# Kernel tuning notes

Measured on AMD Instinct MI355X. Metric: run time of the kernel, lower is better.

The kernel has to match this reference:

```python
import jax, jax.numpy as jnp
import numpy as np

EPS = 1e-5

def _bn(x):
    # training-mode batchnorm (batch stats), gamma=1 beta=0 per the module's init
    ax = tuple(range(x.ndim - 1))
    m = x.mean(ax, keepdims=True)
    v = x.var(ax, keepdims=True)
    return (x - m) * jax.lax.rsqrt(v + EPS)

def _mlp(x, weights):
    # shared 1x1-conv MLP: pointwise linear -> BN -> ReLU
    for W in weights:
        x = jax.nn.relu(_bn(jnp.einsum('...c,oc->...o', x, W)))
    return x

def _fps_single(xyz, npoint):
    # farthest point sampling, xyz [N,3] -> [npoint] int32 indices
    N = xyz.shape[0]
    def step(carry, _):
        dists, far = carry
        d = jnp.sum((xyz - xyz[far]) ** 2, -1)
        dists = jnp.minimum(dists, d)
        return (dists, jnp.argmax(dists).astype(jnp.int32)), far
    init = (jnp.full((N,), 1e10, xyz.dtype), jnp.int32(0))
    _, idx = jax.lax.scan(step, init, None, length=npoint)
    return idx

def _ball_query(new_xyz, xyz, radius, nsample):
    # first nsample points (in original order) within radius of each center
    d2 = jnp.sum((new_xyz[:, :, None, :] - xyz[:, None, :, :]) ** 2, -1)  # [B,S,N]
    N = xyz.shape[1]
    rank = jnp.where(d2 < radius * radius, jnp.arange(N, dtype=jnp.int32), jnp.int32(N))
    vals, _ = jax.lax.top_k(-rank, nsample)
    idx = -vals
    idx = jnp.where(idx == N, idx[..., :1], idx)  # pad with first valid (center itself)
    return idx

def _gather(pts, idx):
    # pts [B,N,C], idx [B,S,ns] -> [B,S,ns,C]
    B, S, ns = idx.shape
    return jnp.take_along_axis(pts, idx.reshape(B, S * ns, 1), axis=1).reshape(B, S, ns, pts.shape[-1])

def _sa(xyz, feats, npoint, radius, nsample, weights):
    fps_idx = jax.vmap(_fps_single, in_axes=(0, None))(xyz, npoint)
    new_xyz = jnp.take_along_axis(xyz, fps_idx[:, :, None], axis=1)  # [B,S,3]
    idx = _ball_query(new_xyz, xyz, radius, nsample)
    g_xyz = (_gather(xyz, idx) - new_xyz[:, :, None, :]) / radius  # normalize_xyz
    x = g_xyz if feats is None else jnp.concatenate([g_xyz, _gather(feats, idx)], -1)
    x = _mlp(x, weights)
    return new_xyz, x.max(axis=2), fps_idx  # maxpool over nsample

def _forward(obj_cloud, gripper_cloud, sa1_w0, sa1_w1, sa1_w2, sa2_w0, sa2_w1, sa2_w2,
             sa3_w0, sa3_w1, sa3_w2, ge_w0, ge_w1, ge_w2,
             head_w0, head_b0, head_w1, head_b1, head_w2, head_b2):
    # gripper encoder: pointwise conv1d MLP + global maxpool
    g = _mlp(gripper_cloud, [ge_w0, ge_w1, ge_w2])      # [B,G,128]
    gripper_feature = g.max(axis=1)                      # [B,128]
    # backbone
    xyz1, f1, _ = _sa(obj_cloud, None, 512, 0.2, 32, [sa1_w0, sa1_w1, sa1_w2])
    xyz2, f2, _ = _sa(xyz1, f1, 128, 0.4, 64, [sa2_w0, sa2_w1, sa2_w2])
    # sa3: group_all (use_xyz, no centering/normalization)
    x = jnp.concatenate([xyz2, f2], -1)[:, None]         # [B,1,128,259]
    x = _mlp(x, [sa3_w0, sa3_w1, sa3_w2])
    obj_feature = x.max(axis=2)[:, 0]                    # [B,1024]
    comb = jnp.concatenate([gripper_feature, obj_feature], -1)  # [B,1152]
    h = _bn(comb)
    h = jax.nn.relu(_bn(h @ head_w0.T + head_b0))
    h = jax.nn.relu(_bn(h @ head_w1.T + head_b1))
    return jax.nn.relu(h @ head_w2.T + head_b2)          # [B,1]

def setup_inputs() -> dict:
    key = jax.random.key(0)
    ks = jax.random.split(key, 24)
    def w(k, o, i):
        return (jax.random.normal(k, (o, i), jnp.float32) * 0.05)
    inp = {
        'obj_cloud': jax.random.uniform(ks[0], (8, 20000, 3), jnp.float32),
        'gripper_cloud': jax.random.uniform(ks[1], (8, 512, 3), jnp.float32),
        'sa1_w0': w(ks[2], 64, 3),   'sa1_w1': w(ks[3], 64, 64),   'sa1_w2': w(ks[4], 128, 64),
        'sa2_w0': w(ks[5], 128, 131),'sa2_w1': w(ks[6], 128, 128), 'sa2_w2': w(ks[7], 256, 128),
        'sa3_w0': w(ks[8], 256, 259),'sa3_w1': w(ks[9], 512, 256), 'sa3_w2': w(ks[10], 1024, 512),
        'ge_w0': w(ks[11], 64, 3),   'ge_w1': w(ks[12], 128, 64),  'ge_w2': w(ks[13], 128, 128),
        'head_w0': w(ks[14], 512, 1152), 'head_b0': jnp.zeros((512,), jnp.float32),
        'head_w1': w(ks[15], 256, 512),  'head_b1': jnp.zeros((256,), jnp.float32),
        'head_w2': w(ks[16], 1, 256),    'head_b2': jnp.zeros((1,), jnp.float32),
    }
    return inp

def reference(obj_cloud, gripper_cloud, sa1_w0, sa1_w1, sa1_w2, sa2_w0, sa2_w1, sa2_w2,
              sa3_w0, sa3_w1, sa3_w2, ge_w0, ge_w1, ge_w2,
              head_w0, head_b0, head_w1, head_b1, head_w2, head_b2):
    return _forward(obj_cloud, gripper_cloud, sa1_w0, sa1_w1, sa1_w2, sa2_w0, sa2_w1, sa2_w2,
                    sa3_w0, sa3_w1, sa3_w2, ge_w0, ge_w1, ge_w2,
                    head_w0, head_b0, head_w1, head_b1, head_w2, head_b2)
```

## Files before the change

### kernel.cpp

```cpp
#include <hip/hip_runtime.h>
#include <cstddef>
#include <cstdint>

#define EPS_BN 1e-5f
#define NBINS 4
#define NEG_INF (-__builtin_inff())

template <bool FUSE_IN, bool FUSE_MAX>
__global__ __launch_bounds__(256) void gemm_xwt(const float* __restrict__ X,
                                                const float* __restrict__ Wm,
                                                float* __restrict__ Y,
                                                int R, int Cin, int Cout,
                                                const float* __restrict__ st_in, int Rin,
                                                float* __restrict__ st_out,
                                                float* __restrict__ pooled, int ns) {
  __shared__ __align__(16) float Xs[16][132];
  __shared__ __align__(16) float Ws[16][132];
  __shared__ float sMean[512], sScale[512];
  const int t  = threadIdx.x;
  const int r0 = blockIdx.x << 7;
  const int n0 = blockIdx.y << 7;
  const int tx = t & 15;
  const int ty = t >> 4;

  if constexpr (FUSE_IN) {
    const float inv = 1.f / (float)Rin;
    for (int k = t; k < Cin; k += 256) {
      float s = 0.f, q = 0.f;
#pragma unroll
      for (int bn = 0; bn < NBINS; ++bn) {
        s += st_in[bn * 2 * Cin + k];
        q += st_in[bn * 2 * Cin + Cin + k];
      }
      const float m  = s * inv;
      const float vr = fmaf(-m, m, q * inv);
      sMean[k]  = m;
      sScale[k] = rsqrtf(vr + EPS_BN);
    }
    __syncthreads();
  }

  float acc[8][8] = {};
  const int rStage = t >> 1;
  const int kBase  = (t & 1) << 3;
  const int nr     = n0 + rStage;

  for (int k0 = 0; k0 < Cin; k0 += 16) {
    const float* xrow = X  + (size_t)(r0 + rStage) * Cin + k0 + kBase;
    const float* wrow = Wm + (size_t)nr * Cin + k0 + kBase;
    if (((Cin & 3) == 0) && (k0 + 16 <= Cin)) {
      float4 xa = *(const float4*)(xrow);
      float4 xb = *(const float4*)(xrow + 4);
      if constexpr (FUSE_IN) {
        const int kb = k0 + kBase;
        xa.x = fmaxf(0.f, (xa.x - sMean[kb + 0]) * sScale[kb + 0]);
        xa.y = fmaxf(0.f, (xa.y - sMean[kb + 1]) * sScale[kb + 1]);
        xa.z = fmaxf(0.f, (xa.z - sMean[kb + 2]) * sScale[kb + 2]);
        xa.w = fmaxf(0.f, (xa.w - sMean[kb + 3]) * sScale[kb + 3]);
        xb.x = fmaxf(0.f, (xb.x - sMean[kb + 4]) * sScale[kb + 4]);
        xb.y = fmaxf(0.f, (xb.y - sMean[kb + 5]) * sScale[kb + 5]);
        xb.z = fmaxf(0.f, (xb.z - sMean[kb + 6]) * sScale[kb + 6]);
        xb.w = fmaxf(0.f, (xb.w - sMean[kb + 7]) * sScale[kb + 7]);
      }
      Xs[kBase + 0][rStage] = xa.x; Xs[kBase + 1][rStage] = xa.y;
      Xs[kBase + 2][rStage] = xa.z; Xs[kBase + 3][rStage] = xa.w;
      Xs[kBase + 4][rStage] = xb.x; Xs[kBase + 5][rStage] = xb.y;
      Xs[kBase + 6][rStage] = xb.z; Xs[kBase + 7][rStage] = xb.w;
      float4 wa = {0, 0, 0, 0}, wb = {0, 0, 0, 0};
      if (nr < Cout) { wa = *(const float4*)(wrow); wb = *(const float4*)(wrow + 4); }
      Ws[kBase + 0][rStage] = wa.x; Ws[kBase + 1][rStage] = wa.y;
      Ws[kBase + 2][rStage] = wa.z; Ws[kBase + 3][rStage] = wa.w;
      Ws[kBase + 4][rStage] = wb.x; Ws[kBase + 5][rStage] = wb.y;
      Ws[kBase + 6][rStage] = wb.z; Ws[kBase + 7][rStage] = wb.w;
    } else {
#pragma unroll
      for (int u = 0; u < 8; ++u) {
        const int k = k0 + kBase + u;
        float xe = 0.f, we = 0.f;
        if (k < Cin) {
          xe = xrow[u];
          if constexpr (FUSE_IN) xe = fmaxf(0.f, (xe - sMean[k]) * sScale[k]);
          if (nr < Cout) we = wrow[u];
        }
        Xs[kBase + u][rStage] = xe;
        Ws[kBase + u][rStage] = we;
      }
    }
    __syncthreads();
#pragma unroll
    for (int kk = 0; kk < 16; ++kk) {
      const float4 a0 = *(const float4*)(&Xs[kk][ty << 2]);
      const float4 a1 = *(const float4*)(&Xs[kk][64 + (ty << 2)]);
      const float4 b0 = *(const float4*)(&Ws[kk][tx << 2]);
      const float4 b1 = *(const float4*)(&Ws[kk][64 + (tx << 2)]);
      const float av[8] = {a0.x, a0.y, a0.z, a0.w, a1.x, a1.y, a1.z, a1.w};
      const float bw[8] = {b0.x, b0.y, b0.z, b0.w, b1.x, b1.y, b1.z, b1.w};
#pragma unroll
      for (int i = 0; i < 8; ++i)
#pragma unroll
        for (int j = 0; j < 8; ++j) acc[i][j] = fmaf(av[i], bw[j], acc[i][j]);
    }
    __syncthreads();
  }
  if constexpr (!FUSE_MAX) {
#pragma unroll
    for (int h = 0; h < 2; ++h)
#pragma unroll
      for (int i = 0; i < 4; ++i) {
        const int r = r0 + h * 64 + (ty << 2) + i;
        float* yr = Y + (size_t)r * Cout;
#pragma unroll
        for (int g = 0; g < 2; ++g) {
          const int n = n0 + g * 64 + (tx << 2);
          if (n < Cout) {
            float4 o = {acc[h * 4 + i][g * 4 + 0], acc[h * 4 + i][g * 4 + 1],
                        acc[h * 4 + i][g * 4 + 2], acc[h * 4 + i][g * 4 + 3]};
            *(float4*)(yr + n) = o;
          }
        }
      }
  }
#pragma unroll
  for (int g = 0; g < 2; ++g)
#pragma unroll
    for (int j = 0; j < 4; ++j) {
      float s = 0.f, q = 0.f;
#pragma unroll
      for (int rh = 0; rh < 8; ++rh) {
        const float v = acc[rh][g * 4 + j];
        s += v;
        q = fmaf(v, v, q);
      }
      Xs[ty][g * 64 + (tx << 2) + j] = s;
      Ws[ty][g * 64 + (tx << 2) + j] = q;
    }
  __syncthreads();
  if (t < 128) {
    const int n = n0 + t;
    if (n < Cout) {
      float s = 0.f, q = 0.f;
#pragma unroll
      for (int w = 0; w < 16; ++w) { s += Xs[w][t]; q += Ws[w][t]; }
      float* dst = st_out + (blockIdx.x & (NBINS - 1)) * 2 * Cout;
      atomicAdd(dst + n, s);
      atomicAdd(dst + Cout + n, q);
    }
  }
  if constexpr (FUSE_MAX) {
    __syncthreads();
    float mxAll = NEG_INF;
#pragma unroll
    for (int h = 0; h < 2; ++h) {
#pragma unroll
      for (int g2 = 0; g2 < 2; ++g2)
#pragma unroll
        for (int j = 0; j < 4; ++j) {
          float mx = acc[h * 4 + 0][g2 * 4 + j];
          mx = fmaxf(mx, acc[h * 4 + 1][g2 * 4 + j]);
          mx = fmaxf(mx, acc[h * 4 + 2][g2 * 4 + j]);
          mx = fmaxf(mx, acc[h * 4 + 3][g2 * 4 + j]);
          Xs[ty][g2 * 64 + (tx << 2) + j] = mx;
        }
      __syncthreads();
      if (t < 128) {
        const int n = n0 + t;
        if (n < Cout) {
          if (ns <= 64) {
            const int tpg = ns >> 2;
            const int gph = 64 / ns;
            for (int gq = 0; gq < gph; ++gq) {
              float mx = NEG_INF;
              for (int w = gq * tpg; w < gq * tpg + tpg; ++w) mx = fmaxf(mx, Xs[w][t]);
              const int g = (r0 + h * 64) / ns + gq;
              pooled[(size_t)g * Cout + n] = mx;
            }
          } else {
            float mx = NEG_INF;
            for (int w = 0; w < 16; ++w) mx = fmaxf(mx, Xs[w][t]);
            mxAll = fmaxf(mxAll, mx);
          }
        }
      }
      __syncthreads();
    }
    if (ns > 64 && t < 128) {
      const int n = n0 + t;
      if (n < Cout) pooled[(size_t)(r0 >> 7) * Cout + n] = mxAll;
    }
  }
}

__global__ void bn_apply_pooled(const float* __restrict__ P, const float* __restrict__ st,
                                float* __restrict__ o, int G, int C, int Rtrue) {
  const int i = blockIdx.x * 256 + threadIdx.x;
  if (i >= G * C) return;
  const int c = i % C;
  float s = 0.f, q = 0.f;
#pragma unroll
  for (int bn = 0; bn < NBINS; ++bn) {
    s += st[bn * 2 * C + c];
    q += st[bn * 2 * C + C + c];
  }
  const float inv = 1.f / (float)Rtrue;
  const float m  = s * inv;
  const float vr = fmaf(-m, m, q * inv);
  const float sc = rsqrtf(vr + EPS_BN);
  o[i] = fmaxf(0.f, (P[i] - m) * sc);
}

__global__ void bn_apply_relu_maxpool(const float* __restrict__ Y,
                                      const float* __restrict__ st,
                                      float* __restrict__ o, int G, int ns, int C) {
  const int i = blockIdx.x * 256 + threadIdx.x;
  if (i >= G * C) return;
  const int c = i % C;
  const int g = i / C;
  float s = 0.f, q = 0.f;
#pragma unroll
  for (int bn = 0; bn < NBINS; ++bn) {
    s += st[bn * 2 * C + c];
    q += st[bn * 2 * C + C + c];
  }
  const int R = G * ns;
  const float inv = 1.f / (float)R;
  const float m  = s * inv;
  const float vr = fmaf(-m, m, q * inv);
  const float sc = rsqrtf(vr + EPS_BN);
  const float* p = Y + (size_t)g * ns * C + c;
  float mx = NEG_INF;
  for (int k = 0; k < ns; ++k) mx = fmaxf(mx, p[(size_t)k * C]);
  o[i] = fmaxf(0.f, (mx - m) * sc);
}

#define REP20(X) X(0) X(1) X(2) X(3) X(4) X(5) X(6) X(7) X(8) X(9) \
                 X(10) X(11) X(12) X(13) X(14) X(15) X(16) X(17) X(18) X(19)

__global__ __launch_bounds__(1024)
__attribute__((amdgpu_waves_per_eu(4, 4)))
void fps_sa1_kernel(const float* __restrict__ xyz, float* __restrict__ new_xyz) {
  const int b    = blockIdx.x;
  const int tid  = threadIdx.x;
  const int lane = tid & 63;
  const int wave = tid >> 6;
  const float* p = xyz + (size_t)b * 20000 * 3;

  __shared__ float sv[16], sx[16], sy[16], sz[16];
  __shared__ int   si[16];
  __shared__ float bc[3];

#define DECLR(k) float px##k, py##k, pz##k, dd##k;
  REP20(DECLR)
#undef DECLR

#define INITR(k) {                                                          \
    const int i = tid + ((k) << 10);                                        \
    if (i < 20000) {                                                        \
      px##k = p[i * 3 + 0]; py##k = p[i * 3 + 1]; pz##k = p[i * 3 + 2];     \
      dd##k = 1e10f;                                                        \
    } else {                                                                \
      px##k = 0.f; py##k = 0.f; pz##k = 0.f;                                \
      dd##k = NEG_INF;                                                      \
    } }
  REP20(INITR)
#undef INITR

  float fx = p[0], fy = p[1], fz = p[2];
  if (tid == 0) {
    float* o = new_xyz + (size_t)b * 512 * 3;
    o[0] = fx; o[1] = fy; o[2] = fz;
  }
  __syncthreads();

  for (int s = 1; s < 512; ++s) {
    float bv = NEG_INF;
    int   bi = 0x7fffffff;
    float bx = 0.f, by = 0.f, bz = 0.f;
#define SCANR(k) {                                                          \
    const float dx = px##k - fx, dy = py##k - fy, dz = pz##k - fz;          \
    const float d  = __fadd_rn(__fadd_rn(__fmul_rn(dx, dx), __fmul_rn(dy, dy)), \
                               __fmul_rn(dz, dz));                          \
    const float nd = fminf(dd##k, d);                                       \
    dd##k = nd;                                                             \
    if (nd > bv) { bv = nd; bi = tid + ((k) << 10);                         \
                   bx = px##k; by = py##k; bz = pz##k; } }
    REP20(SCANR)
#undef SCANR
    float v  = bv;
    int   i0 = bi;
#pragma unroll
    for (int m = 1; m < 64; m <<= 1) {
      const float ov = __shfl_xor(v, m, 64);
      const int   oi = __shfl_xor(i0, m, 64);
      if (ov > v || (ov == v && oi < i0)) { v = ov; i0 = oi; }
    }
    if (i0 == bi) {
      sv[wave] = bv; si[wave] = bi; sx[wave] = bx; sy[wave] = by; sz[wave] = bz;
    }
    __syncthreads();
    if (tid < 64) {
      const float lv = (lane < 16) ? sv[lane] : NEG_INF;
      const int   li = (lane < 16) ? si[lane] : 0x7fffffff;
      float v2 = lv;
      int   i2 = li;
#pragma unroll
      for (int m = 1; m < 16; m <<= 1) {
        const float ov = __shfl_xor(v2, m, 64);
        const int   oi = __shfl_xor(i2, m, 64);
        if (ov > v2 || (ov == v2 && oi < i2)) { v2 = ov; i2 = oi; }
      }
      if (lane < 16 && li == i2) {
        const float wx = sx[lane], wy = sy[lane], wz = sz[lane];
        bc[0] = wx; bc[1] = wy; bc[2] = wz;
        float* o = new_xyz + ((size_t)b * 512 + s) * 3;
        o[0] = wx; o[1] = wy; o[2] = wz;
      }
    }
    __syncthreads();
    fx = bc[0]; fy = bc[1]; fz = bc[2];
  }
}

template <int N, int NP, int THREADS, int NPT>
__global__ __launch_bounds__(THREADS)
void fps2_kernel(const float* __restrict__ xyz, float* __restrict__ new_xyz) {
  constexpr int NW = THREADS / 64;
  const int b    = blockIdx.x;
  const int tid  = threadIdx.x;
  const int lane = tid & 63;
  const int wave = tid >> 6;
  const float* p = xyz + (size_t)b * N * 3;
  float px[NPT], py[NPT], pz[NPT], dd[NPT];
#pragma unroll
  for (int j = 0; j < NPT; ++j) {
    const int i = tid + j * THREADS;
    if (i < N) {
      px[j] = p[i * 3 + 0];
      py[j] = p[i * 3 + 1];
      pz[j] = p[i * 3 + 2];
      dd[j] = 1e10f;
    } else {
      px[j] = 0.f; py[j] = 0.f; pz[j] = 0.f;
      dd[j] = NEG_INF;
    }
  }
  __shared__ float sv[NW], sx[NW], sy[NW], sz[NW];
  __shared__ int   si[NW];
  __shared__ float bc[3];
  float fx = p[0], fy = p[1], fz = p[2];
  if (tid == 0) {
    float* o = new_xyz + (size_t)b * NP * 3;
    o[0] = fx; o[1] = fy; o[2] = fz;
  }
  for (int s = 1; s < NP; ++s) {
    float bv = NEG_INF;
    int   bi = 0x7fffffff;
    float bx = 0.f, by = 0.f, bz = 0.f;
#pragma unroll
    for (int j = 0; j < NPT; ++j) {
      const float dx = px[j] - fx;
      const float dy = py[j] - fy;
      const float dz = pz[j] - fz;
      const float d  = __fadd_rn(__fadd_rn(__fmul_rn(dx, dx), __fmul_rn(dy, dy)),
                                 __fmul_rn(dz, dz));
      const float nd = fminf(dd[j], d);
      dd[j] = nd;
      if (nd > bv) { bv = nd; bi = tid + j * THREADS; bx = px[j]; by = py[j]; bz = pz[j]; }
    }
    float v = bv;
    int   i0 = bi;
#pragma unroll
    for (int m = 1; m < 64; m <<= 1) {
      const float ov = __shfl_xor(v, m, 64);
      const int   oi = __shfl_xor(i0, m, 64);
      if (ov > v || (ov == v && oi < i0)) { v = ov; i0 = oi; }
    }
    if (i0 == bi) {
      sv[wave] = bv; si[wave] = bi; sx[wave] = bx; sy[wave] = by; sz[wave] = bz;
    }
    __syncthreads();
    if (tid < 64) {
      const float lv = (lane < NW) ? sv[lane] : NEG_INF;
      const int   li = (lane < NW) ? si[lane] : 0x7fffffff;
      float v2 = lv;
      int   i2 = li;
#pragma unroll
      for (int m = 1; m < NW; m <<= 1) {
        const float ov = __shfl_xor(v2, m, 64);
        const int   oi = __shfl_xor(i2, m, 64);
        if (ov > v2 || (ov == v2 && oi < i2)) { v2 = ov; i2 = oi; }
      }
      if (lane < NW && li == i2) {
        const float wx = sx[lane], wy = sy[lane], wz = sz[lane];
        bc[0] = wx; bc[1] = wy; bc[2] = wz;
        float* o = new_xyz + ((size_t)b * NP + s) * 3;
        o[0] = wx; o[1] = wy; o[2] = wz;
      }
    }
    __syncthreads();
    fx = bc[0]; fy = bc[1]; fz = bc[2];
  }
}

template <int N, int NS>
__global__ __launch_bounds__(256)
void ballquery_wave_kernel(const float* __restrict__ centers,
                           const float* __restrict__ pts,
                           int* __restrict__ idx, int BS, int S, float r2) {
  const int w    = (blockIdx.x * 256 + threadIdx.x) >> 6;
  const int lane = threadIdx.x & 63;
  if (w >= BS) return;
  const int b = w / S;
  const float cx = centers[w * 3 + 0];
  const float cy = centers[w * 3 + 1];
  const float cz = centers[w * 3 + 2];
  const float* p = pts + (size_t)b * N * 3;
  int* o = idx + (size_t)w * NS;
  int total = 0;
  int first = -1;
  for (int i0 = 0; i0 < N && total < NS; i0 += 64) {
    const int i = i0 + lane;
    bool pred = false;
    if (i < N) {
      const float dx = cx - p[i * 3 + 0];
      const float dy = cy - p[i * 3 + 1];
      const float dz = cz - p[i * 3 + 2];
      const float d2 = __fadd_rn(__fadd_rn(__fmul_rn(dx, dx), __fmul_rn(dy, dy)),
                                 __fmul_rn(dz, dz));
      pred = (d2 < r2);
    }
    const unsigned long long mask = __ballot(pred);
    if (mask) {
      const unsigned long long below = (lane == 0) ? 0ull : (mask << (64 - lane));
      const int before = __popcll(below);
      if (pred && (total + before) < NS) o[total + before] = i;
      if (first < 0) first = i0 + (__ffsll((long long)mask) - 1);
      total += __popcll(mask);
    }
  }
  if (lane >= total && lane < NS) o[lane] = first;
}

__global__ void group1_kernel(const float* __restrict__ xyz, const float* __restrict__ ctr,
                              const int* __restrict__ idx, float* __restrict__ X1) {
  const int t = blockIdx.x * 256 + threadIdx.x;
  if (t >= 8 * 512 * 32) return;
  const int g = t >> 5;
  const int b = g >> 9;
  const int i = idx[t];
  const float* p = xyz + ((size_t)b * 20000 + i) * 3;
  const float* c = ctr + (size_t)g * 3;
  X1[t * 3 + 0] = (p[0] - c[0]) / 0.2f;
  X1[t * 3 + 1] = (p[1] - c[1]) / 0.2f;
  X1[t * 3 + 2] = (p[2] - c[2]) / 0.2f;
}

__global__ void group2_kernel(const float* __restrict__ xyz1,
                              const float* __restrict__ xyz2,
                              const float* __restrict__ f1,
                              const int* __restrict__ idx2,
                              float* __restrict__ X2) {
  const int t = blockIdx.x * 256 + threadIdx.x;
  if (t >= 65536 * 131) return;
  const int r = t / 131;
  const int c = t - r * 131;
  const int g = r >> 6;
  const int b = g >> 7;
  const int i = idx2[r];
  float v;
  if (c < 3) {
    v = (xyz1[((size_t)b * 512 + i) * 3 + c] - xyz2[(size_t)g * 3 + c]) / 0.4f;
  } else {
    v = f1[((size_t)b * 512 + i) * 128 + (c - 3)];
  }
  X2[t] = v;
}

__global__ void build_x3_kernel(const float* __restrict__ xyz2, const float* __restrict__ f2,
                                float* __restrict__ X3) {
  const int t = blockIdx.x * 256 + threadIdx.x;
  if (t >= 1024 * 259) return;
  const int r = t / 259;
  const int c = t - r * 259;
  X3[t] = (c < 3) ? xyz2[r * 3 + c] : f2[(size_t)r * 256 + (c - 3)];
}

__global__ __launch_bounds__(512) void head_kernel(
    const float* __restrict__ gfeat, const float* __restrict__ objf,
    const float* __restrict__ w0, const float* __restrict__ b0,
    const float* __restrict__ w1, const float* __restrict__ b1,
    const float* __restrict__ w2, const float* __restrict__ b2,
    float* __restrict__ out) {
  __shared__ __align__(16) float comb[8 * 1152];
  __shared__ __align__(16) float h1[8 * 512];
  __shared__ __align__(16) float h2[8 * 256];
  const int tid = threadIdx.x;
  for (int i = tid; i < 8 * 1152; i += 512) {
    const int b = i / 1152, c = i - b * 1152;
    comb[i] = (c < 128) ? gfeat[b * 128 + c] : objf[b * 1024 + (c - 128)];
  }
  __syncthreads();
  for (int c = tid; c < 1152; c += 512) {
    float s = 0.f;
#pragma unroll
    for (int b = 0; b < 8; ++b) s += comb[b * 1152 + c];
    const float m = s * 0.125f;
    float v = 0.f;
#pragma unroll
    for (int b = 0; b < 8; ++b) { const float d = comb[b * 1152 + c] - m; v = fmaf(d, d, v); }
    const float sc = rsqrtf(v * 0.125f + EPS_BN);
#pragma unroll
    for (int b = 0; b < 8; ++b) comb[b * 1152 + c] = (comb[b * 1152 + c] - m) * sc;
  }
  __syncthreads();
  {
    float a[8];
#pragma unroll
    for (int b = 0; b < 8; ++b) a[b] = b0[tid];
    const float* wr = w0 + (size_t)tid * 1152;
    for (int ci = 0; ci < 1152; ci += 4) {
      const float4 wv = *(const float4*)(wr + ci);
#pragma unroll
      for (int b = 0; b < 8; ++b) {
        const float4 xv = *(const float4*)(&comb[b * 1152 + ci]);
        a[b] = fmaf(xv.x, wv.x, a[b]);
        a[b] = fmaf(xv.y, wv.y, a[b]);
        a[b] = fmaf(xv.z, wv.z, a[b]);
        a[b] = fmaf(xv.w, wv.w, a[b]);
      }
    }
    float s = 0.f;
#pragma unroll
    for (int b = 0; b < 8; ++b) s += a[b];
    const float m = s * 0.125f;
    float v = 0.f;
#pragma unroll
    for (int b = 0; b < 8; ++b) { const float d = a[b] - m; v = fmaf(d, d, v); }
    const float sc = rsqrtf(v * 0.125f + EPS_BN);
#pragma unroll
    for (int b = 0; b < 8; ++b) h1[b * 512 + tid] = fmaxf(0.f, (a[b] - m) * sc);
  }
  __syncthreads();
  if (tid < 256) {
    float a[8];
#pragma unroll
    for (int b = 0; b < 8; ++b) a[b] = b1[tid];
    const float* wr = w1 + (size_t)tid * 512;
    for (int ci = 0; ci < 512; ci += 4) {
      const float4 wv = *(const float4*)(wr + ci);
#pragma unroll
      for (int b = 0; b < 8; ++b) {
        const float4 xv = *(const float4*)(&h1[b * 512 + ci]);
        a[b] = fmaf(xv.x, wv.x, a[b]);
        a[b] = fmaf(xv.y, wv.y, a[b]);
        a[b] = fmaf(xv.z, wv.z, a[b]);
        a[b] = fmaf(xv.w, wv.w, a[b]);
      }
    }
    float s = 0.f;
#pragma unroll
    for (int b = 0; b < 8; ++b) s += a[b];
    const float m = s * 0.125f;
    float v = 0.f;
#pragma unroll
    for (int b = 0; b < 8; ++b) { const float d = a[b] - m; v = fmaf(d, d, v); }
    const float sc = rsqrtf(v * 0.125f + EPS_BN);
#pragma unroll
    for (int b = 0; b < 8; ++b) h2[b * 256 + tid] = fmaxf(0.f, (a[b] - m) * sc);
  }
  __syncthreads();
  if (tid < 8) {
    float s = b2[0];
    for (int ci = 0; ci < 256; ++ci) s = fmaf(h2[tid * 256 + ci], w2[ci], s);
    out[tid] = fmaxf(0.f, s);
  }
}

extern "C" void kernel_launch(void* const* d_in, const int* in_sizes, int n_in,
                              void* d_out, int out_size, void* d_ws, size_t ws_size,
                              hipStream_t stream) {
  (void)in_sizes; (void)n_in; (void)out_size; (void)ws_size;
  const float* obj  = (const float*)d_in[0];
  const float* grip = (const float*)d_in[1];
  const float* s1w0 = (const float*)d_in[2];
  const float* s1w1 = (const float*)d_in[3];
  const float* s1w2 = (const float*)d_in[4];
  const float* s2w0 = (const float*)d_in[5];
  const float* s2w1 = (const float*)d_in[6];
  const float* s2w2 = (const float*)d_in[7];
  const float* s3w0 = (const float*)d_in[8];
  const float* s3w1 = (const float*)d_in[9];
  const float* s3w2 = (const float*)d_in[10];
  const float* gw0  = (const float*)d_in[11];
  const float* gw1  = (const float*)d_in[12];
  const float* gw2  = (const float*)d_in[13];
  const float* hw0  = (const float*)d_in[14];
  const float* hb0  = (const float*)d_in[15];
  const float* hw1  = (const float*)d_in[16];
  const float* hb1  = (const float*)d_in[17];
  const float* hw2  = (const float*)d_in[18];
  const float* hb2  = (const float*)d_in[19];
  float* out = (float*)d_out;

  float* wsf   = (float*)d_ws;
  float* stats = wsf;
  float* xyz1  = wsf + 23040;
  float* xyz2  = wsf + 35328;
  float* gfeat = wsf + 38400;
  float* objf  = wsf + 39424;
  float* f1    = wsf + 47616;
  float* f2    = wsf + 571904;
  float* x3    = wsf + 834048;
  int*   idx1  = (int*)(wsf + 1099264);
  int*   idx2  = (int*)(wsf + 1230336);
  float* bufP  = wsf + 1295872;
  float* bufQ  = wsf + 18073088;

  static const int st_off[12] = {0, 512, 1536, 2560, 3072, 3584,
                                 4608, 5632, 6656, 8704, 10752, 14848};
  auto st = [&](int li) { return stats + st_off[li]; };

  hipMemsetAsync(stats, 0, 23040 * sizeof(float), stream);

  auto gemm0 = [&](const float* X, const float* Wm, float* Y, int R, int Cin, int Cout,
                   int lo) {
    dim3 g((R + 127) / 128, (Cout + 127) / 128);
    gemm_xwt<false, false><<<g, 256, 0, stream>>>(X, Wm, Y, R, Cin, Cout, nullptr, 0,
                                                  st(lo), nullptr, 0);
  };
  auto gemmf = [&](const float* X, const float* Wm, float* Y, int R, int Cin, int Cout,
                   int li, int lo) {
    dim3 g((R + 127) / 128, (Cout + 127) / 128);
    gemm_xwt<true, false><<<g, 256, 0, stream>>>(X, Wm, Y, R, Cin, Cout, st(li), R,
                                                 st(lo), nullptr, 0);
  };
  auto gemmfM = [&](const float* X, const float* Wm, float* pooled, int R, int Cin,
                    int Cout, int li, int lo, int ns) {
    dim3 g((R + 127) / 128, (Cout + 127) / 128);
    gemm_xwt<true, true><<<g, 256, 0, stream>>>(X, Wm, nullptr, R, Cin, Cout, st(li), R,
                                                st(lo), pooled, ns);
  };
  auto applymax_k = [&](const float* Y, int li, int G, int ns, int C, float* o) {
    const int n = G * C;
    bn_apply_relu_maxpool<<<(n + 255) / 256, 256, 0, stream>>>(Y, st(li), o, G, ns, C);
  };
  auto applypool_k = [&](const float* P, int li, int G, int C, int Rtrue, float* o) {
    const int n = G * C;
    bn_apply_pooled<<<(n + 255) / 256, 256, 0, stream>>>(P, st(li), o, G, C, Rtrue);
  };

  fps_sa1_kernel<<<8, 1024, 0, stream>>>(obj, xyz1);

  float* gY1 = bufP;
  float* gY2 = bufP + 262144;
  float* gY3 = bufP + 786432;
  gemm0(grip, gw0, gY1, 4096, 3, 64, 0);
  gemmf(gY1, gw1, gY2, 4096, 64, 128, 0, 1);
  gemmf(gY2, gw2, gY3, 4096, 128, 128, 1, 2);
  applymax_k(gY3, 2, 8, 512, 128, gfeat);

  ballquery_wave_kernel<20000, 32><<<1024, 256, 0, stream>>>(xyz1, obj, idx1, 4096, 512, 0.04f);
  float* X1 = bufQ;
  group1_kernel<<<512, 256, 0, stream>>>(obj, xyz1, idx1, X1);
  gemm0(X1, s1w0, bufP, 131072, 3, 64, 3);
  gemmf(bufP, s1w1, bufQ, 131072, 64, 64, 3, 4);
  gemmfM(bufQ, s1w2, bufP, 131072, 64, 128, 4, 5, 32);
  applypool_k(bufP, 5, 4096, 128, 131072, f1);

  fps2_kernel<512, 128, 256, 2><<<8, 256, 0, stream>>>(xyz1, xyz2);
  ballquery_wave_kernel<512, 64><<<256, 256, 0, stream>>>(xyz2, xyz1, idx2, 1024, 128, 0.16f);
  float* X2 = bufQ;
  group2_kernel<<<(65536 * 131 + 255) / 256, 256, 0, stream>>>(xyz1, xyz2, f1, idx2, X2);
  gemm0(X2, s2w0, bufP, 65536, 131, 128, 6);
  gemmf(bufP, s2w1, bufQ, 65536, 128, 128, 6, 7);
  gemmfM(bufQ, s2w2, bufP, 65536, 128, 256, 7, 8, 64);
  applypool_k(bufP, 8, 1024, 256, 65536, f2);

  build_x3_kernel<<<(1024 * 259 + 255) / 256, 256, 0, stream>>>(xyz2, f2, x3);
  float* Y3a = bufQ;
  float* Y3b = bufQ + 262144;
  float* Y3p = bufQ + 786432;
  gemm0(x3, s3w0, Y3a, 1024, 259, 256, 9);
  gemmf(Y3a, s3w1, Y3b, 1024, 256, 512, 9, 10);
  gemmfM(Y3b, s3w2, Y3p, 1024, 512, 1024, 10, 11, 128);
  applypool_k(Y3p, 11, 8, 1024, 1024, objf);

  head_kernel<<<1, 512, 0, stream>>>(gfeat, objf, hw0, hb0, hw1, hb1, hw2, hb2, out);
}
```

Baseline: 2.349 ms.

## Fuse pooled BN-apply into consumers, merge ball query with grouping, single-wave FPS2

Removes the standalone bn_apply_pooled launches by folding the batch-norm normalize and ReLU of the pooled features into group2, build_x3 and the head kernel, each of which recomputes mean and scale from the stats bins. Merges the SA1 ball query with grouping so the neighbor indices stay in shared memory and no index buffer round-trip is needed. Rewrites the second FPS as a single 64-lane wave that shuffles the winner coordinates, which removes the block barriers from every sampling step. This cuts launches and intermediate buffers. In exchange the consumers repeat the BN math, and group2 redoes it for every gathered element.

```diff
diff --git a/kernel.cpp b/kernel.cpp
--- a/kernel.cpp
+++ b/kernel.cpp
@@ -190,24 +190,6 @@
   }
 }
 
-__global__ void bn_apply_pooled(const float* __restrict__ P, const float* __restrict__ st,
-                                float* __restrict__ o, int G, int C, int Rtrue) {
-  const int i = blockIdx.x * 256 + threadIdx.x;
-  if (i >= G * C) return;
-  const int c = i % C;
-  float s = 0.f, q = 0.f;
-#pragma unroll
-  for (int bn = 0; bn < NBINS; ++bn) {
-    s += st[bn * 2 * C + c];
-    q += st[bn * 2 * C + C + c];
-  }
-  const float inv = 1.f / (float)Rtrue;
-  const float m  = s * inv;
-  const float vr = fmaf(-m, m, q * inv);
-  const float sc = rsqrtf(vr + EPS_BN);
-  o[i] = fmaxf(0.f, (P[i] - m) * sc);
-}
-
 __global__ void bn_apply_relu_maxpool(const float* __restrict__ Y,
                                       const float* __restrict__ st,
                                       float* __restrict__ o, int G, int ns, int C) {
@@ -320,84 +302,52 @@
   }
 }
 
-template <int N, int NP, int THREADS, int NPT>
-__global__ __launch_bounds__(THREADS)
-void fps2_kernel(const float* __restrict__ xyz, float* __restrict__ new_xyz) {
-  constexpr int NW = THREADS / 64;
+__global__ __launch_bounds__(64)
+void fps2_wave_kernel(const float* __restrict__ xyz, float* __restrict__ new_xyz) {
   const int b    = blockIdx.x;
-  const int tid  = threadIdx.x;
-  const int lane = tid & 63;
-  const int wave = tid >> 6;
-  const float* p = xyz + (size_t)b * N * 3;
-  float px[NPT], py[NPT], pz[NPT], dd[NPT];
-#pragma unroll
-  for (int j = 0; j < NPT; ++j) {
-    const int i = tid + j * THREADS;
-    if (i < N) {
-      px[j] = p[i * 3 + 0];
-      py[j] = p[i * 3 + 1];
-      pz[j] = p[i * 3 + 2];
-      dd[j] = 1e10f;
-    } else {
-      px[j] = 0.f; py[j] = 0.f; pz[j] = 0.f;
-      dd[j] = NEG_INF;
-    }
-  }
-  __shared__ float sv[NW], sx[NW], sy[NW], sz[NW];
-  __shared__ int   si[NW];
-  __shared__ float bc[3];
+  const int lane = threadIdx.x;
+  const float* p = xyz + (size_t)b * 512 * 3;
+  float px[8], py[8], pz[8], dd[8];
+#pragma unroll
+  for (int j = 0; j < 8; ++j) {
+    const int i = lane + (j << 6);
+    px[j] = p[i * 3 + 0]; py[j] = p[i * 3 + 1]; pz[j] = p[i * 3 + 2];
+    dd[j] = 1e10f;
+  }
   float fx = p[0], fy = p[1], fz = p[2];
-  if (tid == 0) {
-    float* o = new_xyz + (size_t)b * NP * 3;
+  if (lane == 0) {
+    float* o = new_xyz + (size_t)b * 128 * 3;
     o[0] = fx; o[1] = fy; o[2] = fz;
   }
-  for (int s = 1; s < NP; ++s) {
+  for (int s = 1; s < 128; ++s) {
     float bv = NEG_INF;
     int   bi = 0x7fffffff;
     float bx = 0.f, by = 0.f, bz = 0.f;
 #pragma unroll
-    for (int j = 0; j < NPT; ++j) {
-      const float dx = px[j] - fx;
-      const float dy = py[j] - fy;
-      const float dz = pz[j] - fz;
+    for (int j = 0; j < 8; ++j) {
+      const float dx = px[j] - fx, dy = py[j] - fy, dz = pz[j] - fz;
       const float d  = __fadd_rn(__fadd_rn(__fmul_rn(dx, dx), __fmul_rn(dy, dy)),
                                  __fmul_rn(dz, dz));
       const float nd = fminf(dd[j], d);
       dd[j] = nd;
-      if (nd > bv) { bv = nd; bi = tid + j * THREADS; bx = px[j]; by = py[j]; bz = pz[j]; }
-    }
-    float v = bv;
-    int   i0 = bi;
+      if (nd > bv) { bv = nd; bi = lane + (j << 6); bx = px[j]; by = py[j]; bz = pz[j]; }
+    }
+    float v = bv; int i0 = bi;
+    float wx = bx, wy = by, wz = bz;
 #pragma unroll
     for (int m = 1; m < 64; m <<= 1) {
       const float ov = __shfl_xor(v, m, 64);
       const int   oi = __shfl_xor(i0, m, 64);
-      if (ov > v || (ov == v && oi < i0)) { v = ov; i0 = oi; }
-    }
-    if (i0 == bi) {
-      sv[wave] = bv; si[wave] = bi; sx[wave] = bx; sy[wave] = by; sz[wave] = bz;
-    }
-    __syncthreads();
-    if (tid < 64) {
-      const float lv = (lane < NW) ? sv[lane] : NEG_INF;
-      const int   li = (lane < NW) ? si[lane] : 0x7fffffff;
-      float v2 = lv;
-      int   i2 = li;
-#pragma unroll
-      for (int m = 1; m < NW; m <<= 1) {
-        const float ov = __shfl_xor(v2, m, 64);
-        const int   oi = __shfl_xor(i2, m, 64);
-        if (ov > v2 || (ov == v2 && oi < i2)) { v2 = ov; i2 = oi; }
-      }
-      if (lane < NW && li == i2) {
-        const float wx = sx[lane], wy = sy[lane], wz = sz[lane];
-        bc[0] = wx; bc[1] = wy; bc[2] = wz;
-        float* o = new_xyz + ((size_t)b * NP + s) * 3;
-        o[0] = wx; o[1] = wy; o[2] = wz;
-      }
-    }
-    __syncthreads();
-    fx = bc[0]; fy = bc[1]; fz = bc[2];
+      const float ox = __shfl_xor(wx, m, 64);
+      const float oy = __shfl_xor(wy, m, 64);
+      const float oz = __shfl_xor(wz, m, 64);
+      if (ov > v || (ov == v && oi < i0)) { v = ov; i0 = oi; wx = ox; wy = oy; wz = oz; }
+    }
+    fx = wx; fy = wy; fz = wz;
+    if (lane == 0) {
+      float* o = new_xyz + ((size_t)b * 128 + s) * 3;
+      o[0] = fx; o[1] = fy; o[2] = fz;
+    }
   }
 }
 
@@ -440,26 +390,77 @@
   if (lane >= total && lane < NS) o[lane] = first;
 }
 
-__global__ void group1_kernel(const float* __restrict__ xyz, const float* __restrict__ ctr,
-                              const int* __restrict__ idx, float* __restrict__ X1) {
-  const int t = blockIdx.x * 256 + threadIdx.x;
-  if (t >= 8 * 512 * 32) return;
-  const int g = t >> 5;
-  const int b = g >> 9;
-  const int i = idx[t];
-  const float* p = xyz + ((size_t)b * 20000 + i) * 3;
-  const float* c = ctr + (size_t)g * 3;
-  X1[t * 3 + 0] = (p[0] - c[0]) / 0.2f;
-  X1[t * 3 + 1] = (p[1] - c[1]) / 0.2f;
-  X1[t * 3 + 2] = (p[2] - c[2]) / 0.2f;
-}
-
-__global__ void group2_kernel(const float* __restrict__ xyz1,
-                              const float* __restrict__ xyz2,
-                              const float* __restrict__ f1,
-                              const int* __restrict__ idx2,
-                              float* __restrict__ X2) {
-  const int t = blockIdx.x * 256 + threadIdx.x;
+__global__ __launch_bounds__(256)
+void ballq_group1_kernel(const float* __restrict__ centers,
+                         const float* __restrict__ pts,
+                         float* __restrict__ X1) {
+  __shared__ int sIdx[4][32];
+  const int wIn  = threadIdx.x >> 6;
+  const int w    = (blockIdx.x * 256 + threadIdx.x) >> 6;
+  const int lane = threadIdx.x & 63;
+  if (w >= 4096) return;
+  const int b = w >> 9;
+  const float cx = centers[w * 3 + 0];
+  const float cy = centers[w * 3 + 1];
+  const float cz = centers[w * 3 + 2];
+  const float* p = pts + (size_t)b * 20000 * 3;
+  int total = 0;
+  int first = -1;
+  for (int i0 = 0; i0 < 20000 && total < 32; i0 += 64) {
+    const int i = i0 + lane;
+    bool pred = false;
+    if (i < 20000) {
+      const float dx = cx - p[i * 3 + 0];
+      const float dy = cy - p[i * 3 + 1];
+      const float dz = cz - p[i * 3 + 2];
+      const float d2 = __fadd_rn(__fadd_rn(__fmul_rn(dx, dx), __fmul_rn(dy, dy)),
+                                 __fmul_rn(dz, dz));
+      pred = (d2 < 0.04f);
+    }
+    const unsigned long long mask = __ballot(pred);
+    if (mask) {
+      const unsigned long long below = (lane == 0) ? 0ull : (mask << (64 - lane));
+      const int before = __popcll(below);
+      if (pred && (total + before) < 32) sIdx[wIn][total + before] = i;
+      if (first < 0) first = i0 + (__ffsll((long long)mask) - 1);
+      total += __popcll(mask);
+    }
+  }
+  __builtin_amdgcn_wave_barrier();
+  if (lane < 32) {
+    const int i = (lane < total) ? sIdx[wIn][lane] : first;
+    const float* q = p + (size_t)i * 3;
+    float* o = X1 + ((size_t)w * 32 + lane) * 3;
+    o[0] = (q[0] - cx) / 0.2f;
+    o[1] = (q[1] - cy) / 0.2f;
+    o[2] = (q[2] - cz) / 0.2f;
+  }
+}
+
+__global__ __launch_bounds__(256)
+void group2_kernel(const float* __restrict__ xyz1,
+                   const float* __restrict__ xyz2,
+                   const float* __restrict__ P1,
+                   const float* __restrict__ st,
+                   const int* __restrict__ idx2,
+                   float* __restrict__ X2) {
+  __shared__ float sM[128], sS[128];
+  const int t0 = threadIdx.x;
+  if (t0 < 128) {
+    float s = 0.f, q = 0.f;
+#pragma unroll
+    for (int bn = 0; bn < NBINS; ++bn) {
+      s += st[bn * 256 + t0];
+      q += st[bn * 256 + 128 + t0];
+    }
+    const float inv = 1.f / 131072.f;
+    const float m  = s * inv;
+    const float vr = fmaf(-m, m, q * inv);
+    sM[t0] = m;
+    sS[t0] = rsqrtf(vr + EPS_BN);
+  }
+  __syncthreads();
+  const int t = blockIdx.x * 256 + t0;
   if (t >= 65536 * 131) return;
   const int r = t / 131;
   const int c = t - r * 131;
@@ -470,22 +471,50 @@
   if (c < 3) {
     v = (xyz1[((size_t)b * 512 + i) * 3 + c] - xyz2[(size_t)g * 3 + c]) / 0.4f;
   } else {
-    v = f1[((size_t)b * 512 + i) * 128 + (c - 3)];
+    const int cc = c - 3;
+    v = P1[((size_t)b * 512 + i) * 128 + cc];
+    v = fmaxf(0.f, (v - sM[cc]) * sS[cc]);
   }
   X2[t] = v;
 }
 
-__global__ void build_x3_kernel(const float* __restrict__ xyz2, const float* __restrict__ f2,
-                                float* __restrict__ X3) {
-  const int t = blockIdx.x * 256 + threadIdx.x;
+__global__ __launch_bounds__(256)
+void build_x3_kernel(const float* __restrict__ xyz2, const float* __restrict__ P2,
+                     const float* __restrict__ st, float* __restrict__ X3) {
+  __shared__ float sM[256], sS[256];
+  const int t0 = threadIdx.x;
+  {
+    float s = 0.f, q = 0.f;
+#pragma unroll
+    for (int bn = 0; bn < NBINS; ++bn) {
+      s += st[bn * 512 + t0];
+      q += st[bn * 512 + 256 + t0];
+    }
+    const float inv = 1.f / 65536.f;
+    const float m  = s * inv;
+    const float vr = fmaf(-m, m, q * inv);
+    sM[t0] = m;
+    sS[t0] = rsqrtf(vr + EPS_BN);
+  }
+  __syncthreads();
+  const int t = blockIdx.x * 256 + t0;
   if (t >= 1024 * 259) return;
   const int r = t / 259;
   const int c = t - r * 259;
-  X3[t] = (c < 3) ? xyz2[r * 3 + c] : f2[(size_t)r * 256 + (c - 3)];
+  float v;
+  if (c < 3) {
+    v = xyz2[r * 3 + c];
+  } else {
+    const int cc = c - 3;
+    v = P2[(size_t)r * 256 + cc];
+    v = fmaxf(0.f, (v - sM[cc]) * sS[cc]);
+  }
+  X3[t] = v;
 }
 
 __global__ __launch_bounds__(512) void head_kernel(
-    const float* __restrict__ gfeat, const float* __restrict__ objf,
+    const float* __restrict__ gfeat, const float* __restrict__ Y3p,
+    const float* __restrict__ st11,
     const float* __restrict__ w0, const float* __restrict__ b0,
     const float* __restrict__ w1, const float* __restrict__ b1,
     const float* __restrict__ w2, const float* __restrict__ b2,
@@ -496,7 +525,24 @@
   const int tid = threadIdx.x;
   for (int i = tid; i < 8 * 1152; i += 512) {
     const int b = i / 1152, c = i - b * 1152;
-    comb[i] = (c < 128) ? gfeat[b * 128 + c] : objf[b * 1024 + (c - 128)];
+    float v;
+    if (c < 128) {
+      v = gfeat[b * 128 + c];
+    } else {
+      const int cc = c - 128;
+      float s = 0.f, q = 0.f;
+#pragma unroll
+      for (int bn = 0; bn < NBINS; ++bn) {
+        s += st11[bn * 2048 + cc];
+        q += st11[bn * 2048 + 1024 + cc];
+      }
+      const float inv = 1.f / 1024.f;
+      const float m  = s * inv;
+      const float vr = fmaf(-m, m, q * inv);
+      const float sc = rsqrtf(vr + EPS_BN);
+      v = fmaxf(0.f, (Y3p[b * 1024 + cc] - m) * sc);
+    }
+    comb[i] = v;
   }
   __syncthreads();
   for (int c = tid; c < 1152; c += 512) {
@@ -606,11 +652,7 @@
   float* xyz1  = wsf + 23040;
   float* xyz2  = wsf + 35328;
   float* gfeat = wsf + 38400;
-  float* objf  = wsf + 39424;
-  float* f1    = wsf + 47616;
-  float* f2    = wsf + 571904;
   float* x3    = wsf + 834048;
-  int*   idx1  = (int*)(wsf + 1099264);
   int*   idx2  = (int*)(wsf + 1230336);
   float* bufP  = wsf + 1295872;
   float* bufQ  = wsf + 18073088;
@@ -643,10 +685,6 @@
     const int n = G * C;
     bn_apply_relu_maxpool<<<(n + 255) / 256, 256, 0, stream>>>(Y, st(li), o, G, ns, C);
   };
-  auto applypool_k = [&](const float* P, int li, int G, int C, int Rtrue, float* o) {
-    const int n = G * C;
-    bn_apply_pooled<<<(n + 255) / 256, 256, 0, stream>>>(P, st(li), o, G, C, Rtrue);
-  };
 
   fps_sa1_kernel<<<8, 1024, 0, stream>>>(obj, xyz1);
 
@@ -658,31 +696,28 @@
   gemmf(gY2, gw2, gY3, 4096, 128, 128, 1, 2);
   applymax_k(gY3, 2, 8, 512, 128, gfeat);
 
-  ballquery_wave_kernel<20000, 32><<<1024, 256, 0, stream>>>(xyz1, obj, idx1, 4096, 512, 0.04f);
   float* X1 = bufQ;
-  group1_kernel<<<512, 256, 0, stream>>>(obj, xyz1, idx1, X1);
+  ballq_group1_kernel<<<1024, 256, 0, stream>>>(xyz1, obj, X1);
   gemm0(X1, s1w0, bufP, 131072, 3, 64, 3);
   gemmf(bufP, s1w1, bufQ, 131072, 64, 64, 3, 4);
   gemmfM(bufQ, s1w2, bufP, 131072, 64, 128, 4, 5, 32);
-  applypool_k(bufP, 5, 4096, 128, 131072, f1);
-
-  fps2_kernel<512, 128, 256, 2><<<8, 256, 0, stream>>>(xyz1, xyz2);
+
+  fps2_wave_kernel<<<8, 64, 0, stream>>>(xyz1, xyz2);
   ballquery_wave_kernel<512, 64><<<256, 256, 0, stream>>>(xyz2, xyz1, idx2, 1024, 128, 0.16f);
   float* X2 = bufQ;
-  group2_kernel<<<(65536 * 131 + 255) / 256, 256, 0, stream>>>(xyz1, xyz2, f1, idx2, X2);
+  group2_kernel<<<(65536 * 131 + 255) / 256, 256, 0, stream>>>(xyz1, xyz2, bufP, st(5),
+                                                               idx2, X2);
   gemm0(X2, s2w0, bufP, 65536, 131, 128, 6);
   gemmf(bufP, s2w1, bufQ, 65536, 128, 128, 6, 7);
   gemmfM(bufQ, s2w2, bufP, 65536, 128, 256, 7, 8, 64);
-  applypool_k(bufP, 8, 1024, 256, 65536, f2);
-
-  build_x3_kernel<<<(1024 * 259 + 255) / 256, 256, 0, stream>>>(xyz2, f2, x3);
+
+  build_x3_kernel<<<(1024 * 259 + 255) / 256, 256, 0, stream>>>(xyz2, bufP, st(8), x3);
   float* Y3a = bufQ;
   float* Y3b = bufQ + 262144;
   float* Y3p = bufQ + 786432;
   gemm0(x3, s3w0, Y3a, 1024, 259, 256, 9);
   gemmf(Y3a, s3w1, Y3b, 1024, 256, 512, 9, 10);
   gemmfM(Y3b, s3w2, Y3p, 1024, 512, 1024, 10, 11, 128);
-  applypool_k(Y3p, 11, 8, 1024, 1024, objf);
-
-  head_kernel<<<1, 512, 0, stream>>>(gfeat, objf, hw0, hb0, hw1, hb1, hw2, hb2, out);
-}
+
+  head_kernel<<<1, 512, 0, stream>>>(gfeat, Y3p, st(11), hw0, hb0, hw1, hb1, hw2, hb2, out);
+}
```

Measured after the change: 2.326 ms. No clear change (-1.0%).
